# Optimization experiments

Measured on AMD Instinct MI355X. Metric: run time of the kernel, lower is better.

The kernel has to match this reference:

```python
import jax, jax.numpy as jnp
import numpy as np

CHUNK = 1024  # rows of pc0 processed per tile to avoid materializing the full NxM matrix


def _min_sqdist(a, b):
    """For each row of a [N,3], min squared distance to rows of b [M,3]."""
    b_sq = jnp.sum(b * b, axis=1)  # [M]

    def tile_min(ac):  # ac: [CHUNK, 3]
        d = jnp.sum(ac * ac, axis=1)[:, None] + b_sq[None, :] - 2.0 * (ac @ b.T)
        return jnp.min(d, axis=1)

    n, dim = a.shape
    return jax.lax.map(tile_min, a.reshape(n // CHUNK, CHUNK, dim)).reshape(n)


def setup_inputs() -> dict:
    key = jax.random.key(0)
    k0, k1 = jax.random.split(key)
    pc0 = jax.random.normal(k0, (65536, 3), dtype=jnp.float32)
    pc1 = jax.random.normal(k1, (65536, 3), dtype=jnp.float32)
    return {"pc0": pc0, "pc1": pc1}


def reference(pc0, pc1):
    # chamfer forward: dist0[i] = min_j ||pc0[i]-pc1[j]||^2
    dist0 = _min_sqdist(pc0, pc1)
    mask = dist0 <= 2.0
    # mean over selected elements (boolean mask is constant wrt grads, as in torch)
    return jnp.sum(jnp.where(mask, dist0, 0.0)) / jnp.sum(mask).astype(dist0.dtype)
```

## Files before the change

### kernel.cpp

```cpp
#include <hip/hip_runtime.h>


constexpr int   NPTS  = 65536;
constexpr int   G     = 64;
constexpr int   NC    = G * G * G;
constexpr float H     = 0.125f;
constexpr float ORG   = -4.0f;
constexpr float INVH  = 8.0f;
constexpr int   G3    = 32;
constexpr int   NC3   = G3 * G3 * G3;
constexpr float H3    = 0.25f;
constexpr float INVH3 = 4.0f;
constexpr int   BLOCK = 256;
constexpr int   PBLOCKS = 256;
constexpr int   SB    = 128;
constexpr int   SB3   = 16;
constexpr int   CHUNK = NC / SB;

__device__ __forceinline__ int cellOf(float x) {
  int c = (int)floorf((x - ORG) * INVH);
  return min(max(c, 0), G - 1);
}
__device__ __forceinline__ int cellOf3(float x) {
  int c = (int)floorf((x - ORG) * INVH3);
  return min(max(c, 0), G3 - 1);
}

__global__ __launch_bounds__(BLOCK) void count_kernel(
    const float* __restrict__ pc0, const float* __restrict__ pc1,
    unsigned* __restrict__ counts0, unsigned* __restrict__ counts1,
    unsigned* __restrict__ counts3) {
  const int gid = blockIdx.x * BLOCK + threadIdx.x;
  if (gid < NPTS) {
    const float x = pc1[3 * gid], y = pc1[3 * gid + 1], z = pc1[3 * gid + 2];
    atomicAdd(&counts1[(cellOf(z) * G + cellOf(y)) * G + cellOf(x)], 1u);
    atomicAdd(&counts3[(cellOf3(z) * G3 + cellOf3(y)) * G3 + cellOf3(x)], 1u);
  } else {
    const int i = gid - NPTS;
    const float x = pc0[3 * i], y = pc0[3 * i + 1], z = pc0[3 * i + 2];
    atomicAdd(&counts0[(cellOf(z) * G + cellOf(y)) * G + cellOf(x)], 1u);
  }
}

__global__ __launch_bounds__(1024) void scan_partial_kernel(
    const unsigned* __restrict__ counts0, const unsigned* __restrict__ counts1,
    const unsigned* __restrict__ counts3, unsigned* __restrict__ partials) {
  if (blockIdx.y == 2 && blockIdx.x >= SB3) return;
  const unsigned* counts = (blockIdx.y == 0) ? counts1
                         : (blockIdx.y == 1) ? counts0 : counts3;
  const int base = blockIdx.x * CHUNK + threadIdx.x * 2;
  unsigned sum = counts[base] + counts[base + 1];
  for (int o = 32; o; o >>= 1) sum += __shfl_down(sum, o, 64);
  __shared__ unsigned ws[16];
  if ((threadIdx.x & 63) == 0) ws[threadIdx.x >> 6] = sum;
  __syncthreads();
  if (threadIdx.x == 0) {
    unsigned t = 0;
    for (int w = 0; w < 16; ++w) t += ws[w];
    partials[blockIdx.y * SB + blockIdx.x] = t;
  }
}

__global__ __launch_bounds__(1024) void scan_mid_kernel(
    unsigned* __restrict__ partials) {
  __shared__ unsigned wt[4];
  const int tid = threadIdx.x;
  unsigned v = 0, inc = 0; int g = 0, li = 0;
  if (tid < 256) {
    g = tid >> 7; li = tid & 127;
    v = partials[g * SB + li];
    inc = v;
    for (int o = 1; o < 64; o <<= 1) {
      const unsigned t = __shfl_up(inc, o, 64);
      if ((tid & 63) >= o) inc += t;
    }
    if ((tid & 63) == 63) wt[tid >> 6] = inc;
  } else if (tid < 256 + SB3) {
    v = partials[256 + (tid - 256)];
    inc = v;
    for (int o = 1; o < 16; o <<= 1) {
      const unsigned t = __shfl_up(inc, o, 64);
      if ((tid & 63) >= o) inc += t;
    }
  }
  __syncthreads();
  if (tid < 256) {
    const unsigned woff = ((tid >> 6) & 1) ? wt[g << 1] : 0u;
    partials[g * SB + li] = woff + inc - v;
  } else if (tid < 256 + SB3) {
    partials[256 + (tid - 256)] = inc - v;
  }
}

__global__ __launch_bounds__(1024) void scan_final_kernel(
    const unsigned* __restrict__ counts0, unsigned* __restrict__ cur0,
    const unsigned* __restrict__ counts1, unsigned* __restrict__ cur1,
    const unsigned* __restrict__ counts3, unsigned* __restrict__ cur3,
    const unsigned* __restrict__ partials) {
  if (blockIdx.y == 2 && blockIdx.x >= SB3) return;
  const unsigned* counts = (blockIdx.y == 0) ? counts1
                         : (blockIdx.y == 1) ? counts0 : counts3;
  unsigned* cur          = (blockIdx.y == 0) ? cur1
                         : (blockIdx.y == 1) ? cur0 : cur3;
  const int tid = threadIdx.x;
  const int base = blockIdx.x * CHUNK + tid * 2;
  const unsigned a = counts[base], b = counts[base + 1];
  const unsigned tsum = a + b;
  unsigned inc = tsum;
  for (int o = 1; o < 64; o <<= 1) {
    const unsigned t = __shfl_up(inc, o, 64);
    if ((tid & 63) >= o) inc += t;
  }
  __shared__ unsigned wt[16];
  if ((tid & 63) == 63) wt[tid >> 6] = inc;
  __syncthreads();
  if (tid < 16) {
    unsigned w = wt[tid];
    for (int o = 1; o < 16; o <<= 1) {
      const unsigned t = __shfl_up(w, o, 16);
      if (tid >= o) w += t;
    }
    wt[tid] = w;
  }
  __syncthreads();
  const unsigned woff = (tid >> 6) ? wt[(tid >> 6) - 1] : 0u;
  const unsigned off =
      partials[blockIdx.y * SB + blockIdx.x] + woff + inc - tsum;
  cur[base] = off;
  cur[base + 1] = off + a;
}

__global__ __launch_bounds__(BLOCK) void scatter_kernel(
    const float* __restrict__ pc0, const float* __restrict__ pc1,
    unsigned* __restrict__ cur0, unsigned* __restrict__ cur1,
    unsigned* __restrict__ cur3,
    float4* __restrict__ q, float4* __restrict__ s, float4* __restrict__ s3) {
  const int gid = blockIdx.x * BLOCK + threadIdx.x;
  if (gid < NPTS) {
    const float x = pc1[3 * gid], y = pc1[3 * gid + 1], z = pc1[3 * gid + 2];
    const float4 pt = make_float4(x, y, z, 0.f);
    const int cid  = (cellOf(z) * G + cellOf(y)) * G + cellOf(x);
    const int cid3 = (cellOf3(z) * G3 + cellOf3(y)) * G3 + cellOf3(x);
    s[atomicAdd(&cur1[cid], 1u)] = pt;
    s3[atomicAdd(&cur3[cid3], 1u)] = pt;
  } else {
    const int i = gid - NPTS;
    const float x = pc0[3 * i], y = pc0[3 * i + 1], z = pc0[3 * i + 2];
    const int cid = (cellOf(z) * G + cellOf(y)) * G + cellOf(x);
    q[atomicAdd(&cur0[cid], 1u)] = make_float4(x, y, z, 0.f);
  }
}

__global__ __launch_bounds__(BLOCK) void query_kernel(
    const float4* __restrict__ q, const unsigned* __restrict__ ends,
    const float4* __restrict__ s,
    unsigned* __restrict__ wl, float* __restrict__ wlBest,
    unsigned* __restrict__ pendCnt, float* __restrict__ bkt) {
  const int gtid = blockIdx.x * BLOCK + threadIdx.x;
  const int i   = gtid >> 1;
  const int sub = gtid & 1;
  const float4 p = q[i];
  const int cx = cellOf(p.x), cy = cellOf(p.y), cz = cellOf(p.z);
  const int x0 = max(cx - 1, 0), x1 = min(cx + 1, G - 1);

  unsigned rs[9], re[9];
#pragma unroll
  for (int rr = 0; rr < 9; ++rr) {
    const int zz = cz + rr / 3 - 1, yy = cy + rr % 3 - 1;
    const bool ok = (zz >= 0) && (zz < G) && (yy >= 0) && (yy < G);
    const int rb = ok ? (zz * G + yy) * G : 0;
    rs[rr] = ok ? ((rb + x0) ? ends[rb + x0 - 1] : 0u) : 0u;
    re[rr] = ok ? ends[rb + x1] : 0u;
  }
  float best = 3.4e38f;
#pragma unroll
  for (int rr = 0; rr < 9; ++rr) {
#pragma unroll 4
    for (unsigned j = rs[rr] + sub; j < re[rr]; j += 2) {
      const float4 c = s[j];
      const float dx = p.x - c.x, dy = p.y - c.y, dz = p.z - c.z;
      best = fminf(best, fmaf(dx, dx, fmaf(dy, dy, dz * dz)));
    }
  }
  best = fminf(best, __shfl_xor(best, 1, 64));

  float v = 0.f, c = 0.f;
  if (sub == 0) {
    if (best > H * H) {
      const unsigned k = atomicAdd(pendCnt, 1u);
      wl[k] = (unsigned)i; wlBest[k] = best;
    } else if (best <= 2.0f) { v = best; c = 1.0f; }
  }

  for (int o = 32; o; o >>= 1) {
    v += __shfl_down(v, o, 64);
    c += __shfl_down(c, o, 64);
  }
  __shared__ float wsum[BLOCK / 64], wcnt[BLOCK / 64];
  const int wid = threadIdx.x >> 6;
  if ((threadIdx.x & 63) == 0) { wsum[wid] = v; wcnt[wid] = c; }
  __syncthreads();
  if (threadIdx.x == 0) {
    float bv = 0.f, bc = 0.f;
    for (int w = 0; w < BLOCK / 64; ++w) { bv += wsum[w]; bc += wcnt[w]; }
    if (bc != 0.f) {
      atomicAdd(&bkt[2 * (blockIdx.x & 63) + 0], bv);
      atomicAdd(&bkt[2 * (blockIdx.x & 63) + 1], bc);
    }
  }
}

__global__ __launch_bounds__(BLOCK) void pending_kernel(
    const float4* __restrict__ q,
    const unsigned* __restrict__ ends3, const float4* __restrict__ s3,
    const unsigned* __restrict__ wl, const float* __restrict__ wlBest,
    unsigned* __restrict__ pendCnt, float* __restrict__ bkt,
    unsigned* __restrict__ done, float* __restrict__ out) {
  __shared__ int snP;
  __shared__ float wsum[BLOCK / 64], wcnt[BLOCK / 64];
  __shared__ int isLast;
  __shared__ float fs[BLOCK / 64], fc[BLOCK / 64];
  if (threadIdx.x == 0) snP = (int)atomicAdd(pendCnt, 0u);
  __syncthreads();
  const int lane = threadIdx.x & 63, wid = threadIdx.x >> 6;
  const int gw = blockIdx.x * (BLOCK / 64) + wid;
  const int nW = PBLOCKS * (BLOCK / 64);
  float v = 0.f, c = 0.f;

  for (int it = gw; it < snP; it += nW) {
    const unsigned qi = wl[it];
    const float4 p = q[qi];
    const int cx = cellOf3(p.x), cy = cellOf3(p.y), cz = cellOf3(p.z);
    float best = wlBest[it];

    for (int r = 1; r <= 8; ++r) {
      const float cov = H3 * (float)(r - 1);
      if (best <= cov * cov) break;
      if (best > 2.0f && cov * cov >= 2.0f) break;
      const int S = (r == 1) ? 9 : 8 * r + 2 * (2 * r - 1) * (2 * r - 1);
      float b = best;
      for (int sI = lane; sI < S; sI += 64) {
        int dz, dy, xa, xb;
        if (r == 1) {
          dz = sI / 3 - 1; dy = sI % 3 - 1; xa = cx - 1; xb = cx + 1;
        } else if (sI < 8 * r) {
          if (sI < 2 * r + 1)      { dz = -r; dy = sI - r; }
          else if (sI < 4 * r + 2) { dz =  r; dy = sI - (2 * r + 1) - r; }
          else { const int t2 = sI - (4 * r + 2); dz = (t2 >> 1) - (r - 1);
                 dy = (t2 & 1) ? r : -r; }
          xa = cx - r; xb = cx + r;
        } else {
          const int t2 = sI - 8 * r, ci = t2 >> 1, w1 = 2 * r - 1;
          dz = ci / w1 - (r - 1); dy = ci % w1 - (r - 1);
          xa = xb = (t2 & 1) ? cx + r : cx - r;
        }
        const int zz = cz + dz, yy = cy + dy;
        if (zz < 0 || zz >= G3 || yy < 0 || yy >= G3) continue;
        const int a = max(xa, 0), e = min(xb, G3 - 1);
        if (a > e) continue;
        const int rb = (zz * G3 + yy) * G3;
        const unsigned js = (rb + a) ? ends3[rb + a - 1] : 0u;
        const unsigned je = ends3[rb + e];
        for (unsigned j = js; j < je; ++j) {
          const float4 cd = s3[j];
          const float dx = p.x - cd.x, dyv = p.y - cd.y, dzv = p.z - cd.z;
          b = fminf(b, fmaf(dx, dx, fmaf(dyv, dyv, dzv * dzv)));
        }
      }
      for (int o = 32; o; o >>= 1) b = fminf(b, __shfl_xor(b, o, 64));
      best = b;
    }
    if (lane == 0 && best <= 2.0f) { v += best; c += 1.0f; }
  }

  if (lane == 0) { wsum[wid] = v; wcnt[wid] = c; }
  __syncthreads();
  if (threadIdx.x == 0) {
    float bv = 0.f, bc = 0.f;
    for (int w = 0; w < BLOCK / 64; ++w) { bv += wsum[w]; bc += wcnt[w]; }
    if (bc != 0.f) {
      atomicAdd(&bkt[2 * (blockIdx.x & 63) + 0], bv);
      atomicAdd(&bkt[2 * (blockIdx.x & 63) + 1], bc);
    }
    __threadfence();
    isLast = (atomicAdd(done, 1u) == (unsigned)(PBLOCKS - 1));
  }
  __syncthreads();
  if (isLast) {
    const float val = (threadIdx.x < 128) ? atomicAdd(&bkt[threadIdx.x], 0.0f) : 0.0f;
    float sv = (threadIdx.x & 1) ? 0.f : val;
    float cv = (threadIdx.x & 1) ? val : 0.f;
    for (int o = 32; o; o >>= 1) {
      sv += __shfl_down(sv, o, 64);
      cv += __shfl_down(cv, o, 64);
    }
    if (lane == 0) { fs[wid] = sv; fc[wid] = cv; }
    __syncthreads();
    if (threadIdx.x == 0) {
      float S = 0.f, C = 0.f;
      for (int w = 0; w < BLOCK / 64; ++w) { S += fs[w]; C += fc[w]; }
      out[0] = S / C;
    }
  }
}

extern "C" void kernel_launch(void* const* d_in, const int* in_sizes, int n_in,
                              void* d_out, int out_size, void* d_ws, size_t ws_size,
                              hipStream_t stream) {
  const float* pc0 = (const float*)d_in[0];
  const float* pc1 = (const float*)d_in[1];
  float* out = (float*)d_out;

  char* w = (char*)d_ws;
  auto nxt = [&](size_t bytes) {
    char* p = w; w += (bytes + 255) & ~(size_t)255; return p;
  };
  unsigned* counts1  = (unsigned*)nxt((size_t)NC * 4);
  unsigned* counts0  = (unsigned*)nxt((size_t)NC * 4);
  unsigned* counts3  = (unsigned*)nxt((size_t)NC3 * 4);
  char*     misc     = nxt(1024);
  float*    bkt      = (float*)misc;
  unsigned* done     = (unsigned*)(misc + 512);
  unsigned* pendCnt  = (unsigned*)(misc + 516);
  unsigned* partials = (unsigned*)nxt((size_t)(2 * SB + SB3) * 4);
  unsigned* cur1     = (unsigned*)nxt((size_t)NC * 4);
  unsigned* cur0     = (unsigned*)nxt((size_t)NC * 4);
  unsigned* cur3     = (unsigned*)nxt((size_t)NC3 * 4);
  float4*   s        = (float4*)nxt((size_t)NPTS * 16);
  float4*   s3       = (float4*)nxt((size_t)NPTS * 16);
  float4*   q        = (float4*)nxt((size_t)NPTS * 16);
  unsigned* wl       = (unsigned*)nxt((size_t)NPTS * 4);
  float*    wlBest   = (float*)nxt((size_t)NPTS * 4);

  hipMemsetAsync(counts1, 0, (size_t)2 * NC * 4 + (size_t)NC3 * 4 + 1024, stream);

  count_kernel<<<2 * NPTS / BLOCK, BLOCK, 0, stream>>>(pc0, pc1,
                                                       counts0, counts1, counts3);
  scan_partial_kernel<<<dim3(SB, 3), 1024, 0, stream>>>(counts0, counts1,
                                                        counts3, partials);
  scan_mid_kernel<<<1, 1024, 0, stream>>>(partials);
  scan_final_kernel<<<dim3(SB, 3), 1024, 0, stream>>>(counts0, cur0,
                                                      counts1, cur1,
                                                      counts3, cur3, partials);
  scatter_kernel<<<2 * NPTS / BLOCK, BLOCK, 0, stream>>>(
      pc0, pc1, cur0, cur1, cur3, q, s, s3);
  query_kernel<<<2 * NPTS / BLOCK, BLOCK, 0, stream>>>(q, cur1, s, wl, wlBest,
                                                       pendCnt, bkt);
  pending_kernel<<<PBLOCKS, BLOCK, 0, stream>>>(q, cur3, s3, wl, wlBest,
                                                pendCnt, bkt, done, out);
}
```

Before: 157.2 us.

## Fuse all stages into one cooperative persistent kernel with grid syncs

Replaces the memset and seven separate kernel launches (count, three scan passes, scatter, query, pending) with a single cooperative kernel of 512 blocks. Stages are separated by grid.sync() and the buffer zeroing happens in-kernel. The scan is re-partitioned so each block scans 1024 cells. This removes per-launch overhead and inter-kernel gaps, but adds grid-wide barrier costs. It also limits the pending stage to a fixed grid, and a grid this size must be co-resident to launch.

```diff
diff --git a/kernel.cpp b/kernel.cpp
--- a/kernel.cpp
+++ b/kernel.cpp
@@ -1,4 +1,7 @@
 #include <hip/hip_runtime.h>
+#include <hip/hip_cooperative_groups.h>
+
+namespace cg = cooperative_groups;
 
 
 constexpr int   NPTS  = 65536;
@@ -12,10 +15,7 @@
 constexpr float H3    = 0.25f;
 constexpr float INVH3 = 4.0f;
 constexpr int   BLOCK = 256;
-constexpr int   PBLOCKS = 256;
-constexpr int   SB    = 128;
-constexpr int   SB3   = 16;
-constexpr int   CHUNK = NC / SB;
+constexpr int   GRIDX = 512;
 
 __device__ __forceinline__ int cellOf(float x) {
   int c = (int)floorf((x - ORG) * INVH);
@@ -26,11 +26,30 @@
   return min(max(c, 0), G3 - 1);
 }
 
-__global__ __launch_bounds__(BLOCK) void count_kernel(
+__global__ __launch_bounds__(BLOCK) void mega_kernel(
     const float* __restrict__ pc0, const float* __restrict__ pc1,
     unsigned* __restrict__ counts0, unsigned* __restrict__ counts1,
-    unsigned* __restrict__ counts3) {
-  const int gid = blockIdx.x * BLOCK + threadIdx.x;
+    unsigned* __restrict__ counts3, unsigned* __restrict__ partials,
+    unsigned* __restrict__ cur0, unsigned* __restrict__ cur1,
+    unsigned* __restrict__ cur3,
+    float4* __restrict__ q, float4* __restrict__ s, float4* __restrict__ s3,
+    unsigned* __restrict__ wl, float* __restrict__ wlBest,
+    unsigned* __restrict__ pendCnt, float* __restrict__ bkt,
+    float* __restrict__ out, uint4* __restrict__ zbase, unsigned zvecs) {
+  cg::grid_group grid = cg::this_grid();
+  const int tid  = threadIdx.x;
+  const int bid  = blockIdx.x;
+  const int gid  = bid * BLOCK + tid;
+  const int lane = tid & 63, wid = tid >> 6;
+
+  __shared__ unsigned su[16];
+  __shared__ float    sf[8];
+  __shared__ int      snP;
+
+  for (unsigned i = gid; i < zvecs; i += GRIDX * BLOCK)
+    zbase[i] = make_uint4(0u, 0u, 0u, 0u);
+  grid.sync();
+
   if (gid < NPTS) {
     const float x = pc1[3 * gid], y = pc1[3 * gid + 1], z = pc1[3 * gid + 2];
     atomicAdd(&counts1[(cellOf(z) * G + cellOf(y)) * G + cellOf(x)], 1u);
@@ -40,267 +59,222 @@
     const float x = pc0[3 * i], y = pc0[3 * i + 1], z = pc0[3 * i + 2];
     atomicAdd(&counts0[(cellOf(z) * G + cellOf(y)) * G + cellOf(x)], 1u);
   }
-}
-
-__global__ __launch_bounds__(1024) void scan_partial_kernel(
-    const unsigned* __restrict__ counts0, const unsigned* __restrict__ counts1,
-    const unsigned* __restrict__ counts3, unsigned* __restrict__ partials) {
-  if (blockIdx.y == 2 && blockIdx.x >= SB3) return;
-  const unsigned* counts = (blockIdx.y == 0) ? counts1
-                         : (blockIdx.y == 1) ? counts0 : counts3;
-  const int base = blockIdx.x * CHUNK + threadIdx.x * 2;
-  unsigned sum = counts[base] + counts[base + 1];
-  for (int o = 32; o; o >>= 1) sum += __shfl_down(sum, o, 64);
-  __shared__ unsigned ws[16];
-  if ((threadIdx.x & 63) == 0) ws[threadIdx.x >> 6] = sum;
-  __syncthreads();
-  if (threadIdx.x == 0) {
-    unsigned t = 0;
-    for (int w = 0; w < 16; ++w) t += ws[w];
-    partials[blockIdx.y * SB + blockIdx.x] = t;
-  }
-}
-
-__global__ __launch_bounds__(1024) void scan_mid_kernel(
-    unsigned* __restrict__ partials) {
-  __shared__ unsigned wt[4];
-  const int tid = threadIdx.x;
-  unsigned v = 0, inc = 0; int g = 0, li = 0;
-  if (tid < 256) {
-    g = tid >> 7; li = tid & 127;
-    v = partials[g * SB + li];
-    inc = v;
+  grid.sync();
+
+  {
+    const unsigned* cnt = (bid < 256) ? counts1 : counts0;
+    const int cb = (bid & 255) * 1024 + tid * 4;
+    unsigned sum = cnt[cb] + cnt[cb + 1] + cnt[cb + 2] + cnt[cb + 3];
+    for (int o = 32; o; o >>= 1) sum += __shfl_down(sum, o, 64);
+    if (lane == 0) su[wid] = sum;
+    __syncthreads();
+    if (tid == 0) partials[bid] = su[0] + su[1] + su[2] + su[3];
+    __syncthreads();
+    if (bid < 256) {
+      unsigned v3 = (tid < 128) ? counts3[bid * 128 + tid] : 0u;
+      for (int o = 32; o; o >>= 1) v3 += __shfl_down(v3, o, 64);
+      if (lane == 0 && wid < 2) su[8 + wid] = v3;
+      __syncthreads();
+      if (tid == 0) partials[512 + bid] = su[8] + su[9];
+    }
+  }
+  grid.sync();
+
+  if (bid == 0) {
+    for (int a = 0; a < 3; ++a) {
+      const int off = a * 256;
+      const unsigned v = partials[off + tid];
+      unsigned inc = v;
+      for (int o = 1; o < 64; o <<= 1) {
+        const unsigned t = __shfl_up(inc, o, 64);
+        if (lane >= o) inc += t;
+      }
+      if (lane == 63) su[wid] = inc;
+      __syncthreads();
+      const unsigned woff = (wid >= 1 ? su[0] : 0u) + (wid >= 2 ? su[1] : 0u) +
+                            (wid >= 3 ? su[2] : 0u);
+      partials[off + tid] = woff + inc - v;
+      __syncthreads();
+    }
+  }
+  grid.sync();
+
+  {
+    const unsigned* cnt = (bid < 256) ? counts1 : counts0;
+    unsigned* cur       = (bid < 256) ? cur1 : cur0;
+    const int cb = (bid & 255) * 1024 + tid * 4;
+    const unsigned c0 = cnt[cb], c1 = cnt[cb + 1], c2 = cnt[cb + 2], c3 = cnt[cb + 3];
+    const unsigned tsum = c0 + c1 + c2 + c3;
+    unsigned inc = tsum;
     for (int o = 1; o < 64; o <<= 1) {
       const unsigned t = __shfl_up(inc, o, 64);
-      if ((tid & 63) >= o) inc += t;
-    }
-    if ((tid & 63) == 63) wt[tid >> 6] = inc;
-  } else if (tid < 256 + SB3) {
-    v = partials[256 + (tid - 256)];
-    inc = v;
-    for (int o = 1; o < 16; o <<= 1) {
-      const unsigned t = __shfl_up(inc, o, 64);
-      if ((tid & 63) >= o) inc += t;
-    }
-  }
-  __syncthreads();
-  if (tid < 256) {
-    const unsigned woff = ((tid >> 6) & 1) ? wt[g << 1] : 0u;
-    partials[g * SB + li] = woff + inc - v;
-  } else if (tid < 256 + SB3) {
-    partials[256 + (tid - 256)] = inc - v;
-  }
-}
-
-__global__ __launch_bounds__(1024) void scan_final_kernel(
-    const unsigned* __restrict__ counts0, unsigned* __restrict__ cur0,
-    const unsigned* __restrict__ counts1, unsigned* __restrict__ cur1,
-    const unsigned* __restrict__ counts3, unsigned* __restrict__ cur3,
-    const unsigned* __restrict__ partials) {
-  if (blockIdx.y == 2 && blockIdx.x >= SB3) return;
-  const unsigned* counts = (blockIdx.y == 0) ? counts1
-                         : (blockIdx.y == 1) ? counts0 : counts3;
-  unsigned* cur          = (blockIdx.y == 0) ? cur1
-                         : (blockIdx.y == 1) ? cur0 : cur3;
-  const int tid = threadIdx.x;
-  const int base = blockIdx.x * CHUNK + tid * 2;
-  const unsigned a = counts[base], b = counts[base + 1];
-  const unsigned tsum = a + b;
-  unsigned inc = tsum;
-  for (int o = 1; o < 64; o <<= 1) {
-    const unsigned t = __shfl_up(inc, o, 64);
-    if ((tid & 63) >= o) inc += t;
-  }
-  __shared__ unsigned wt[16];
-  if ((tid & 63) == 63) wt[tid >> 6] = inc;
-  __syncthreads();
-  if (tid < 16) {
-    unsigned w = wt[tid];
-    for (int o = 1; o < 16; o <<= 1) {
-      const unsigned t = __shfl_up(w, o, 16);
-      if (tid >= o) w += t;
-    }
-    wt[tid] = w;
-  }
-  __syncthreads();
-  const unsigned woff = (tid >> 6) ? wt[(tid >> 6) - 1] : 0u;
-  const unsigned off =
-      partials[blockIdx.y * SB + blockIdx.x] + woff + inc - tsum;
-  cur[base] = off;
-  cur[base + 1] = off + a;
-}
-
-__global__ __launch_bounds__(BLOCK) void scatter_kernel(
-    const float* __restrict__ pc0, const float* __restrict__ pc1,
-    unsigned* __restrict__ cur0, unsigned* __restrict__ cur1,
-    unsigned* __restrict__ cur3,
-    float4* __restrict__ q, float4* __restrict__ s, float4* __restrict__ s3) {
-  const int gid = blockIdx.x * BLOCK + threadIdx.x;
+      if (lane >= o) inc += t;
+    }
+    if (lane == 63) su[wid] = inc;
+    __syncthreads();
+    const unsigned woff = (wid >= 1 ? su[0] : 0u) + (wid >= 2 ? su[1] : 0u) +
+                          (wid >= 3 ? su[2] : 0u);
+    unsigned off = partials[bid] + woff + inc - tsum;
+    cur[cb] = off; cur[cb + 1] = off + c0;
+    cur[cb + 2] = off + c0 + c1; cur[cb + 3] = off + c0 + c1 + c2;
+    __syncthreads();
+    if (bid < 256) {
+      unsigned v3 = (tid < 128) ? counts3[bid * 128 + tid] : 0u;
+      unsigned inc3 = v3;
+      for (int o = 1; o < 64; o <<= 1) {
+        const unsigned t = __shfl_up(inc3, o, 64);
+        if (lane >= o) inc3 += t;
+      }
+      if (lane == 63 && wid < 2) su[8 + wid] = inc3;
+      __syncthreads();
+      if (tid < 128) {
+        const unsigned woff3 = (wid == 1) ? su[8] : 0u;
+        cur3[bid * 128 + tid] = partials[512 + bid] + woff3 + inc3 - v3;
+      }
+    }
+  }
+  grid.sync();
+
   if (gid < NPTS) {
     const float x = pc1[3 * gid], y = pc1[3 * gid + 1], z = pc1[3 * gid + 2];
     const float4 pt = make_float4(x, y, z, 0.f);
-    const int cid  = (cellOf(z) * G + cellOf(y)) * G + cellOf(x);
-    const int cid3 = (cellOf3(z) * G3 + cellOf3(y)) * G3 + cellOf3(x);
-    s[atomicAdd(&cur1[cid], 1u)] = pt;
-    s3[atomicAdd(&cur3[cid3], 1u)] = pt;
+    s[atomicAdd(&cur1[(cellOf(z) * G + cellOf(y)) * G + cellOf(x)], 1u)] = pt;
+    s3[atomicAdd(&cur3[(cellOf3(z) * G3 + cellOf3(y)) * G3 + cellOf3(x)], 1u)] = pt;
   } else {
     const int i = gid - NPTS;
     const float x = pc0[3 * i], y = pc0[3 * i + 1], z = pc0[3 * i + 2];
-    const int cid = (cellOf(z) * G + cellOf(y)) * G + cellOf(x);
-    q[atomicAdd(&cur0[cid], 1u)] = make_float4(x, y, z, 0.f);
-  }
-}
-
-__global__ __launch_bounds__(BLOCK) void query_kernel(
-    const float4* __restrict__ q, const unsigned* __restrict__ ends,
-    const float4* __restrict__ s,
-    unsigned* __restrict__ wl, float* __restrict__ wlBest,
-    unsigned* __restrict__ pendCnt, float* __restrict__ bkt) {
-  const int gtid = blockIdx.x * BLOCK + threadIdx.x;
-  const int i   = gtid >> 1;
-  const int sub = gtid & 1;
-  const float4 p = q[i];
-  const int cx = cellOf(p.x), cy = cellOf(p.y), cz = cellOf(p.z);
-  const int x0 = max(cx - 1, 0), x1 = min(cx + 1, G - 1);
-
-  unsigned rs[9], re[9];
+    q[atomicAdd(&cur0[(cellOf(z) * G + cellOf(y)) * G + cellOf(x)], 1u)] =
+        make_float4(x, y, z, 0.f);
+  }
+  grid.sync();
+
+  {
+    const int i = gid >> 1, sub = gid & 1;
+    const float4 p = q[i];
+    const int cx = cellOf(p.x), cy = cellOf(p.y), cz = cellOf(p.z);
+    const int x0 = max(cx - 1, 0), x1 = min(cx + 1, G - 1);
+    unsigned rs[9], re[9];
 #pragma unroll
-  for (int rr = 0; rr < 9; ++rr) {
-    const int zz = cz + rr / 3 - 1, yy = cy + rr % 3 - 1;
-    const bool ok = (zz >= 0) && (zz < G) && (yy >= 0) && (yy < G);
-    const int rb = ok ? (zz * G + yy) * G : 0;
-    rs[rr] = ok ? ((rb + x0) ? ends[rb + x0 - 1] : 0u) : 0u;
-    re[rr] = ok ? ends[rb + x1] : 0u;
-  }
-  float best = 3.4e38f;
+    for (int rr = 0; rr < 9; ++rr) {
+      const int zz = cz + rr / 3 - 1, yy = cy + rr % 3 - 1;
+      const bool ok = (zz >= 0) && (zz < G) && (yy >= 0) && (yy < G);
+      const int rb = ok ? (zz * G + yy) * G : 0;
+      rs[rr] = ok ? ((rb + x0) ? cur1[rb + x0 - 1] : 0u) : 0u;
+      re[rr] = ok ? cur1[rb + x1] : 0u;
+    }
+    float best = 3.4e38f;
 #pragma unroll
-  for (int rr = 0; rr < 9; ++rr) {
+    for (int rr = 0; rr < 9; ++rr) {
 #pragma unroll 4
-    for (unsigned j = rs[rr] + sub; j < re[rr]; j += 2) {
-      const float4 c = s[j];
-      const float dx = p.x - c.x, dy = p.y - c.y, dz = p.z - c.z;
-      best = fminf(best, fmaf(dx, dx, fmaf(dy, dy, dz * dz)));
-    }
-  }
-  best = fminf(best, __shfl_xor(best, 1, 64));
-
-  float v = 0.f, c = 0.f;
-  if (sub == 0) {
-    if (best > H * H) {
-      const unsigned k = atomicAdd(pendCnt, 1u);
-      wl[k] = (unsigned)i; wlBest[k] = best;
-    } else if (best <= 2.0f) { v = best; c = 1.0f; }
-  }
-
-  for (int o = 32; o; o >>= 1) {
-    v += __shfl_down(v, o, 64);
-    c += __shfl_down(c, o, 64);
-  }
-  __shared__ float wsum[BLOCK / 64], wcnt[BLOCK / 64];
-  const int wid = threadIdx.x >> 6;
-  if ((threadIdx.x & 63) == 0) { wsum[wid] = v; wcnt[wid] = c; }
-  __syncthreads();
-  if (threadIdx.x == 0) {
-    float bv = 0.f, bc = 0.f;
-    for (int w = 0; w < BLOCK / 64; ++w) { bv += wsum[w]; bc += wcnt[w]; }
-    if (bc != 0.f) {
-      atomicAdd(&bkt[2 * (blockIdx.x & 63) + 0], bv);
-      atomicAdd(&bkt[2 * (blockIdx.x & 63) + 1], bc);
-    }
-  }
-}
-
-__global__ __launch_bounds__(BLOCK) void pending_kernel(
-    const float4* __restrict__ q,
-    const unsigned* __restrict__ ends3, const float4* __restrict__ s3,
-    const unsigned* __restrict__ wl, const float* __restrict__ wlBest,
-    unsigned* __restrict__ pendCnt, float* __restrict__ bkt,
-    unsigned* __restrict__ done, float* __restrict__ out) {
-  __shared__ int snP;
-  __shared__ float wsum[BLOCK / 64], wcnt[BLOCK / 64];
-  __shared__ int isLast;
-  __shared__ float fs[BLOCK / 64], fc[BLOCK / 64];
-  if (threadIdx.x == 0) snP = (int)atomicAdd(pendCnt, 0u);
-  __syncthreads();
-  const int lane = threadIdx.x & 63, wid = threadIdx.x >> 6;
-  const int gw = blockIdx.x * (BLOCK / 64) + wid;
-  const int nW = PBLOCKS * (BLOCK / 64);
-  float v = 0.f, c = 0.f;
-
-  for (int it = gw; it < snP; it += nW) {
-    const unsigned qi = wl[it];
-    const float4 p = q[qi];
-    const int cx = cellOf3(p.x), cy = cellOf3(p.y), cz = cellOf3(p.z);
-    float best = wlBest[it];
-
-    for (int r = 1; r <= 8; ++r) {
-      const float cov = H3 * (float)(r - 1);
-      if (best <= cov * cov) break;
-      if (best > 2.0f && cov * cov >= 2.0f) break;
-      const int S = (r == 1) ? 9 : 8 * r + 2 * (2 * r - 1) * (2 * r - 1);
-      float b = best;
-      for (int sI = lane; sI < S; sI += 64) {
-        int dz, dy, xa, xb;
-        if (r == 1) {
-          dz = sI / 3 - 1; dy = sI % 3 - 1; xa = cx - 1; xb = cx + 1;
-        } else if (sI < 8 * r) {
-          if (sI < 2 * r + 1)      { dz = -r; dy = sI - r; }
-          else if (sI < 4 * r + 2) { dz =  r; dy = sI - (2 * r + 1) - r; }
-          else { const int t2 = sI - (4 * r + 2); dz = (t2 >> 1) - (r - 1);
-                 dy = (t2 & 1) ? r : -r; }
-          xa = cx - r; xb = cx + r;
-        } else {
-          const int t2 = sI - 8 * r, ci = t2 >> 1, w1 = 2 * r - 1;
-          dz = ci / w1 - (r - 1); dy = ci % w1 - (r - 1);
-          xa = xb = (t2 & 1) ? cx + r : cx - r;
+      for (unsigned j = rs[rr] + sub; j < re[rr]; j += 2) {
+        const float4 c = s[j];
+        const float dx = p.x - c.x, dy = p.y - c.y, dz = p.z - c.z;
+        best = fminf(best, fmaf(dx, dx, fmaf(dy, dy, dz * dz)));
+      }
+    }
+    best = fminf(best, __shfl_xor(best, 1, 64));
+
+    float v = 0.f, c = 0.f;
+    if (sub == 0) {
+      if (best > H * H) {
+        const unsigned k = atomicAdd(pendCnt, 1u);
+        wl[k] = (unsigned)i; wlBest[k] = best;
+      } else if (best <= 2.0f) { v = best; c = 1.0f; }
+    }
+    for (int o = 32; o; o >>= 1) {
+      v += __shfl_down(v, o, 64);
+      c += __shfl_down(c, o, 64);
+    }
+    if (lane == 0) { sf[wid] = v; sf[4 + wid] = c; }
+    __syncthreads();
+    if (tid == 0) {
+      const float bv = sf[0] + sf[1] + sf[2] + sf[3];
+      const float bc = sf[4] + sf[5] + sf[6] + sf[7];
+      if (bc != 0.f) {
+        atomicAdd(&bkt[2 * (bid & 63) + 0], bv);
+        atomicAdd(&bkt[2 * (bid & 63) + 1], bc);
+      }
+    }
+  }
+  grid.sync();
+
+  {
+    if (tid == 0) snP = (int)atomicAdd(pendCnt, 0u);
+    __syncthreads();
+    const int gw = bid * (BLOCK / 64) + wid;
+    const int nW = GRIDX * (BLOCK / 64);
+    float v = 0.f, c = 0.f;
+    for (int it = gw; it < snP; it += nW) {
+      const unsigned qi = wl[it];
+      const float4 p = q[qi];
+      const int cx = cellOf3(p.x), cy = cellOf3(p.y), cz = cellOf3(p.z);
+      float best = wlBest[it];
+      for (int r = 1; r <= 8; ++r) {
+        const float cov = H3 * (float)(r - 1);
+        if (best <= cov * cov) break;
+        if (best > 2.0f && cov * cov >= 2.0f) break;
+        const int S = (r == 1) ? 9 : 8 * r + 2 * (2 * r - 1) * (2 * r - 1);
+        float b = best;
+        for (int sI = lane; sI < S; sI += 64) {
+          int dz, dy, xa, xb;
+          if (r == 1) {
+            dz = sI / 3 - 1; dy = sI % 3 - 1; xa = cx - 1; xb = cx + 1;
+          } else if (sI < 8 * r) {
+            if (sI < 2 * r + 1)      { dz = -r; dy = sI - r; }
+            else if (sI < 4 * r + 2) { dz =  r; dy = sI - (2 * r + 1) - r; }
+            else { const int t2 = sI - (4 * r + 2); dz = (t2 >> 1) - (r - 1);
+                   dy = (t2 & 1) ? r : -r; }
+            xa = cx - r; xb = cx + r;
+          } else {
+            const int t2 = sI - 8 * r, ci = t2 >> 1, w1 = 2 * r - 1;
+            dz = ci / w1 - (r - 1); dy = ci % w1 - (r - 1);
+            xa = xb = (t2 & 1) ? cx + r : cx - r;
+          }
+          const int zz = cz + dz, yy = cy + dy;
+          if (zz < 0 || zz >= G3 || yy < 0 || yy >= G3) continue;
+          const int a = max(xa, 0), e = min(xb, G3 - 1);
+          if (a > e) continue;
+          const int rb = (zz * G3 + yy) * G3;
+          const unsigned js = (rb + a) ? cur3[rb + a - 1] : 0u;
+          const unsigned je = cur3[rb + e];
+          for (unsigned j = js; j < je; ++j) {
+            const float4 cd = s3[j];
+            const float dx = p.x - cd.x, dyv = p.y - cd.y, dzv = p.z - cd.z;
+            b = fminf(b, fmaf(dx, dx, fmaf(dyv, dyv, dzv * dzv)));
+          }
         }
-        const int zz = cz + dz, yy = cy + dy;
-        if (zz < 0 || zz >= G3 || yy < 0 || yy >= G3) continue;
-        const int a = max(xa, 0), e = min(xb, G3 - 1);
-        if (a > e) continue;
-        const int rb = (zz * G3 + yy) * G3;
-        const unsigned js = (rb + a) ? ends3[rb + a - 1] : 0u;
-        const unsigned je = ends3[rb + e];
-        for (unsigned j = js; j < je; ++j) {
-          const float4 cd = s3[j];
-          const float dx = p.x - cd.x, dyv = p.y - cd.y, dzv = p.z - cd.z;
-          b = fminf(b, fmaf(dx, dx, fmaf(dyv, dyv, dzv * dzv)));
-        }
-      }
-      for (int o = 32; o; o >>= 1) b = fminf(b, __shfl_xor(b, o, 64));
-      best = b;
-    }
-    if (lane == 0 && best <= 2.0f) { v += best; c += 1.0f; }
-  }
-
-  if (lane == 0) { wsum[wid] = v; wcnt[wid] = c; }
-  __syncthreads();
-  if (threadIdx.x == 0) {
-    float bv = 0.f, bc = 0.f;
-    for (int w = 0; w < BLOCK / 64; ++w) { bv += wsum[w]; bc += wcnt[w]; }
-    if (bc != 0.f) {
-      atomicAdd(&bkt[2 * (blockIdx.x & 63) + 0], bv);
-      atomicAdd(&bkt[2 * (blockIdx.x & 63) + 1], bc);
-    }
-    __threadfence();
-    isLast = (atomicAdd(done, 1u) == (unsigned)(PBLOCKS - 1));
-  }
-  __syncthreads();
-  if (isLast) {
-    const float val = (threadIdx.x < 128) ? atomicAdd(&bkt[threadIdx.x], 0.0f) : 0.0f;
-    float sv = (threadIdx.x & 1) ? 0.f : val;
-    float cv = (threadIdx.x & 1) ? val : 0.f;
+        for (int o = 32; o; o >>= 1) b = fminf(b, __shfl_xor(b, o, 64));
+        best = b;
+      }
+      if (lane == 0 && best <= 2.0f) { v += best; c += 1.0f; }
+    }
+    __syncthreads();
+    if (lane == 0) { sf[wid] = v; sf[4 + wid] = c; }
+    __syncthreads();
+    if (tid == 0) {
+      const float bv = sf[0] + sf[1] + sf[2] + sf[3];
+      const float bc = sf[4] + sf[5] + sf[6] + sf[7];
+      if (bc != 0.f) {
+        atomicAdd(&bkt[2 * (bid & 63) + 0], bv);
+        atomicAdd(&bkt[2 * (bid & 63) + 1], bc);
+      }
+    }
+  }
+  grid.sync();
+
+  if (bid == 0) {
+    const float val = (tid < 128) ? atomicAdd(&bkt[tid], 0.0f) : 0.0f;
+    float sv = (tid & 1) ? 0.f : val;
+    float cv = (tid & 1) ? val : 0.f;
     for (int o = 32; o; o >>= 1) {
       sv += __shfl_down(sv, o, 64);
       cv += __shfl_down(cv, o, 64);
     }
-    if (lane == 0) { fs[wid] = sv; fc[wid] = cv; }
-    __syncthreads();
-    if (threadIdx.x == 0) {
-      float S = 0.f, C = 0.f;
-      for (int w = 0; w < BLOCK / 64; ++w) { S += fs[w]; C += fc[w]; }
-      out[0] = S / C;
-    }
+    __syncthreads();
+    if (lane == 0) { sf[wid] = sv; sf[4 + wid] = cv; }
+    __syncthreads();
+    if (tid == 0)
+      out[0] = (sf[0] + sf[1] + sf[2] + sf[3]) / (sf[4] + sf[5] + sf[6] + sf[7]);
   }
 }
 
@@ -320,9 +294,8 @@
   unsigned* counts3  = (unsigned*)nxt((size_t)NC3 * 4);
   char*     misc     = nxt(1024);
   float*    bkt      = (float*)misc;
-  unsigned* done     = (unsigned*)(misc + 512);
-  unsigned* pendCnt  = (unsigned*)(misc + 516);
-  unsigned* partials = (unsigned*)nxt((size_t)(2 * SB + SB3) * 4);
+  unsigned* pendCnt  = (unsigned*)(misc + 512);
+  unsigned* partials = (unsigned*)nxt((size_t)768 * 4);
   unsigned* cur1     = (unsigned*)nxt((size_t)NC * 4);
   unsigned* cur0     = (unsigned*)nxt((size_t)NC * 4);
   unsigned* cur3     = (unsigned*)nxt((size_t)NC3 * 4);
@@ -332,20 +305,12 @@
   unsigned* wl       = (unsigned*)nxt((size_t)NPTS * 4);
   float*    wlBest   = (float*)nxt((size_t)NPTS * 4);
 
-  hipMemsetAsync(counts1, 0, (size_t)2 * NC * 4 + (size_t)NC3 * 4 + 1024, stream);
-
-  count_kernel<<<2 * NPTS / BLOCK, BLOCK, 0, stream>>>(pc0, pc1,
-                                                       counts0, counts1, counts3);
-  scan_partial_kernel<<<dim3(SB, 3), 1024, 0, stream>>>(counts0, counts1,
-                                                        counts3, partials);
-  scan_mid_kernel<<<1, 1024, 0, stream>>>(partials);
-  scan_final_kernel<<<dim3(SB, 3), 1024, 0, stream>>>(counts0, cur0,
-                                                      counts1, cur1,
-                                                      counts3, cur3, partials);
-  scatter_kernel<<<2 * NPTS / BLOCK, BLOCK, 0, stream>>>(
-      pc0, pc1, cur0, cur1, cur3, q, s, s3);
-  query_kernel<<<2 * NPTS / BLOCK, BLOCK, 0, stream>>>(q, cur1, s, wl, wlBest,
-                                                       pendCnt, bkt);
-  pending_kernel<<<PBLOCKS, BLOCK, 0, stream>>>(q, cur3, s3, wl, wlBest,
-                                                pendCnt, bkt, done, out);
+  uint4*   zbase = (uint4*)counts1;
+  unsigned zvecs = (unsigned)(((size_t)2 * NC * 4 + (size_t)NC3 * 4 + 1024) / 16);
+
+  void* args[] = {&pc0, &pc1, &counts0, &counts1, &counts3, &partials,
+                  &cur0, &cur1, &cur3, &q, &s, &s3, &wl, &wlBest,
+                  &pendCnt, &bkt, &out, &zbase, &zvecs};
+  hipLaunchCooperativeKernel((void*)mega_kernel, dim3(GRIDX), dim3(BLOCK),
+                             args, 0, stream);
 }
```

After: 569.3 us. +262.1%, slower.
